# Optimization experiments

Measured on AMD Instinct MI355X. Metric: run time of the kernel, lower is better.

## Reference

```python
import jax, jax.numpy as jnp
import numpy as np

B, L, P, K, D, H = 8192, 224, 6, 5, 128, 4
S = K * K                 # 25 spatial positions in the patch
CENTER = S // 2           # central target pixel index
SCALE_RANGE = 0.2
BN_EPS = 1e-5


def _uniform(k, shape, fan_in):
    s = 1.0 / np.sqrt(fan_in)
    return jax.random.uniform(k, shape, jnp.float32, -s, s)


def setup_inputs() -> dict:
    key = jax.random.key(0)
    ks = jax.random.split(key, 32)
    inp = {}
    inp["x"] = jax.random.normal(ks[0], (B, L, K, K), jnp.float32)
    # attention projections (stored as (in, out), applied as x @ W + b)
    inp["wk_w"] = _uniform(ks[1], (L, D), L); inp["wk_b"] = _uniform(ks[2], (D,), L)
    inp["wv_w"] = _uniform(ks[3], (L, D), L); inp["wv_b"] = _uniform(ks[4], (D,), L)
    inp["wq_w"] = _uniform(ks[5], (L, D), L); inp["wq_b"] = _uniform(ks[6], (D,), L)
    inp["ng_w"] = _uniform(ks[7], (D, 1), D); inp["ng_b"] = _uniform(ks[8], (1,), D)
    # ffn branch: GLU(128->64) -> BN -> GLU(64->P)
    inp["f1_fw"] = _uniform(ks[9], (D, 64), D);  inp["f1_fb"] = _uniform(ks[10], (64,), D)
    inp["f1_gw"] = _uniform(ks[11], (D, 64), D); inp["f1_gb"] = _uniform(ks[12], (64,), D)
    inp["f_bn_g"] = jnp.ones((64,), jnp.float32); inp["f_bn_b"] = jnp.zeros((64,), jnp.float32)
    inp["f2_fw"] = _uniform(ks[13], (64, P), 64); inp["f2_fb"] = _uniform(ks[14], (P,), 64)
    inp["f2_gw"] = _uniform(ks[15], (64, P), 64); inp["f2_gb"] = _uniform(ks[16], (P,), 64)
    # scalar branch: same shapes
    inp["s1_fw"] = _uniform(ks[17], (D, 64), D);  inp["s1_fb"] = _uniform(ks[18], (64,), D)
    inp["s1_gw"] = _uniform(ks[19], (D, 64), D);  inp["s1_gb"] = _uniform(ks[20], (64,), D)
    inp["s_bn_g"] = jnp.ones((64,), jnp.float32); inp["s_bn_b"] = jnp.zeros((64,), jnp.float32)
    inp["s2_fw"] = _uniform(ks[21], (64, P), 64); inp["s2_fb"] = _uniform(ks[22], (P,), 64)
    inp["s2_gw"] = _uniform(ks[23], (64, P), 64); inp["s2_gb"] = _uniform(ks[24], (P,), 64)
    # endmember spectra (P, L), nonnegative as typical for HSI
    inp["endmember"] = jax.random.uniform(ks[25], (P, L), jnp.float32)
    return inp


def _swish(x):
    return x * jax.nn.sigmoid(x)


def _glu(x, fw, fb, gw, gb):
    return (x @ fw + fb) * jax.nn.sigmoid(x @ gw + gb)


def _bn_train(x, g, b):
    # BatchNorm1d training-mode forward: biased batch stats over batch dim
    m = jnp.mean(x, axis=0)
    v = jnp.var(x, axis=0)
    return (x - m) * jax.lax.rsqrt(v + BN_EPS) * g + b


def _forward(x, wk_w, wk_b, wv_w, wv_b, wq_w, wq_b, ng_w, ng_b,
             f1_fw, f1_fb, f1_gw, f1_gb, f_bn_g, f_bn_b, f2_fw, f2_fb, f2_gw, f2_gb,
             s1_fw, s1_fb, s1_gw, s1_gb, s_bn_g, s_bn_b, s2_fw, s2_fb, s2_gw, s2_gb,
             endmember):
    b = x.shape[0]
    xt = x.reshape(b, L, S).transpose(0, 2, 1)        # (B, S, L)
    keys = xt @ wk_w + wk_b                            # (B, S, D)
    vals = xt @ wv_w + wv_b                            # (B, S, D)
    q = xt[:, CENTER] @ wq_w + wq_b                    # (B, D)
    dk, dv = D // H, D // H
    kh = keys.reshape(b, S, H, dk)
    qh = q.reshape(b, H, dk)
    # note: scaling uses full key_dim (np.sqrt(self.key_dim)), not per-head dim
    scores = jnp.einsum('bhd,bshd->bhs', qh, kh) / np.sqrt(D).astype(np.float32)
    mask = jnp.zeros((S,), jnp.float32).at[CENTER].set(-1e6)
    att = jax.nn.softmax(scores + mask, axis=-1)       # (B, H, S)
    vh = vals.reshape(b, S, H, dv)
    surround = jnp.einsum('bhs,bshd->bhd', att, vh).reshape(b, D)
    central = vals[:, CENTER]                          # (B, D)
    nearby = jax.nn.sigmoid((central - surround) @ ng_w + ng_b)  # (B, 1)
    ss = central + nearby * surround                   # (B, D) spatial-spectral feature

    h = _glu(_swish(ss), f1_fw, f1_fb, f1_gw, f1_gb)
    h = _swish(_bn_train(h, f_bn_g, f_bn_b))
    abd = jax.nn.softmax(_glu(h, f2_fw, f2_fb, f2_gw, f2_gb), axis=1)  # (B, P)

    g = _glu(_swish(ss), s1_fw, s1_fb, s1_gw, s1_gb)
    g = _swish(_bn_train(g, s_bn_g, s_bn_b))
    edm_scale = jnp.tanh(_glu(g, s2_fw, s2_fb, s2_gw, s2_gb))          # (B, P)

    scale = 1.0 + SCALE_RANGE * edm_scale[:, :, None]  # (B, P, 1)
    edm = scale * endmember[None]                      # (B, P, L)
    recon = jnp.einsum('bp,bpl->bl', abd, edm)         # (B, L)
    return recon, abd, edm_scale


def reference(x, wk_w, wk_b, wv_w, wv_b, wq_w, wq_b, ng_w, ng_b,
              f1_fw, f1_fb, f1_gw, f1_gb, f_bn_g, f_bn_b, f2_fw, f2_fb, f2_gw, f2_gb,
              s1_fw, s1_fb, s1_gw, s1_gb, s_bn_g, s_bn_b, s2_fw, s2_fb, s2_gw, s2_gb,
              endmember):
    return _forward(x, wk_w, wk_b, wv_w, wv_b, wq_w, wq_b, ng_w, ng_b,
                    f1_fw, f1_fb, f1_gw, f1_gb, f_bn_g, f_bn_b, f2_fw, f2_fb, f2_gw, f2_gb,
                    s1_fw, s1_fb, s1_gw, s1_gb, s_bn_g, s_bn_b, s2_fw, s2_fb, s2_gw, s2_gb,
                    endmember)
```

## Files before the change

kernel.cpp:

```cpp
#include <hip/hip_runtime.h>
#include <hip/hip_bf16.h>

typedef unsigned short ushort;
typedef unsigned int   uint;
typedef __bf16 bfrag_t __attribute__((ext_vector_type(8)));
typedef float  ffrag_t __attribute__((ext_vector_type(4)));

#define NB   8192
#define LL   224
#define SS   25
#define CTR  12
#define DD   128
#define PP   6
#define HID  64
#define GPB  2
#define NKC  7
#define NMT  4
#define NNT  24
#define VST  132
#define VBASE (GPB * SS * VST)
#define WPK_ELEMS (NKC * NNT * 64 * 8)
#define FC1_ELEMS (4 * 16 * 64 * 8)

__device__ __forceinline__ float f_sigmoid(float x) { return 1.0f / (1.0f + __expf(-x)); }
__device__ __forceinline__ ushort f2bf(float f) {
    __hip_bfloat16 h = __float2bfloat16(f);
    ushort u; __builtin_memcpy(&u, &h, 2); return u;
}
__device__ __forceinline__ float bfu2f(ushort u) {
    uint v = ((uint)u) << 16; float f; __builtin_memcpy(&f, &v, 4); return f;
}

__global__ __launch_bounds__(256) void k0_pack(
    const float* __restrict__ wk_w, const float* __restrict__ wv_w,
    const float* __restrict__ wq_w,
    const float* __restrict__ f1_fw, const float* __restrict__ f1_gw,
    const float* __restrict__ s1_fw, const float* __restrict__ s1_gw,
    ushort* __restrict__ wpack, ushort* __restrict__ fc1pack,
    float* __restrict__ stats)
{
    const int blk = blockIdx.x;
    if (blk == 0) stats[threadIdx.x] = 0.f;
    if (blk < NNT) {
        const int nt  = blk;
        const int mat = nt >> 3;
        const float* w = mat == 0 ? wk_w : (mat == 1 ? wv_w : wq_w);
        const int cb = (nt & 7) * 16;
        for (int e = threadIdx.x; e < NKC * 64 * 8; e += 256) {
            int j    = e & 7;
            int lane = (e >> 3) & 63;
            int kc   = e >> 9;
            int k = kc * 32 + ((lane >> 4) << 3) + j;
            int c = cb + (lane & 15);
            wpack[((kc * NNT + nt) * 64 + lane) * 8 + j] = f2bf(w[k * DD + c]);
        }
    } else {
        const int nt = blk - NNT;
        const int m2 = nt >> 2;
        const float* w = m2 == 0 ? f1_fw : (m2 == 1 ? f1_gw : (m2 == 2 ? s1_fw : s1_gw));
        const int cb = (nt & 3) * 16;
        for (int e = threadIdx.x; e < 4 * 64 * 8; e += 256) {
            int j    = e & 7;
            int lane = (e >> 3) & 63;
            int kc   = e >> 9;
            int k = kc * 32 + ((lane >> 4) << 3) + j;
            int c = cb + (lane & 15);
            fc1pack[((kc * 16 + nt) * 64 + lane) * 8 + j] = f2bf(w[k * HID + c]);
        }
    }
}

__global__ __launch_bounds__(512, 4) void kA_front(
    const float* __restrict__ x,
    const ushort* __restrict__ wpack,
    const float* __restrict__ wk_b, const float* __restrict__ wv_b,
    const float* __restrict__ wq_b,
    const float* __restrict__ ng_w, const float* __restrict__ ng_b,
    ushort* __restrict__ swv_ws)
{
    __shared__ ushort alds[NMT * NKC * 64 * 8];
    __shared__ float  qv[GPB * DD];
    __shared__ float  att[8 * 26];
    __shared__ float  red[4];

    const int t    = threadIdx.x;
    const int b0   = blockIdx.x * GPB;
    const int wave = t >> 6;
    const int lane = t & 63;

    const int cC = wave * 16 + (lane & 15);
    const float biask = wk_b[cC];
    const float biasv = wv_b[cC];
    const float biasq = wq_b[cC];
    const float ngw   = ng_w[t & 127];

    const float4* xb4 = (const float4*)(x + (size_t)b0 * (LL * SS));
    float4 xf[6];
#pragma unroll
    for (int k = 0; k < 6; ++k) {
        int q = t + k * 512;
        if (q < 2800) xf[k] = xb4[q];
    }
#pragma unroll
    for (int k = 0; k < 6; ++k) {
        int q = t + k * 512;
        if (q < 2800) {
            int e0 = q * 4;
            int g  = e0 >= 5600;
            int eb0 = e0 - g * 5600;
            int l0 = eb0 / 25;
            int s0 = eb0 - l0 * 25;
#pragma unroll
            for (int c = 0; c < 4; ++c) {
                int s = s0 + c;
                int l = l0;
                if (s >= 25) { s -= 25; ++l; }
                int r = g * 32 + s;
                int idx = (((r >> 4) * NKC + (l >> 5)) * 64 +
                           ((r & 15) | (((l >> 3) & 3) << 4))) * 8 + (l & 7);
                float fv = c == 0 ? xf[k].x : c == 1 ? xf[k].y : c == 2 ? xf[k].z : xf[k].w;
                alds[idx] = f2bf(fv);
            }
        }
    }
    __syncthreads();

    ffrag_t acck[NMT], accv[NMT], accq[2];
#pragma unroll
    for (int mt = 0; mt < NMT; ++mt) {
        acck[mt] = ffrag_t{0.f, 0.f, 0.f, 0.f};
        accv[mt] = ffrag_t{0.f, 0.f, 0.f, 0.f};
    }
    accq[0] = ffrag_t{0.f, 0.f, 0.f, 0.f};
    accq[1] = ffrag_t{0.f, 0.f, 0.f, 0.f};

    bfrag_t bk = *(const bfrag_t*)(wpack + ((0 * NNT + wave) * 64 + lane) * 8);
    bfrag_t bv = *(const bfrag_t*)(wpack + ((0 * NNT + wave + 8) * 64 + lane) * 8);
    bfrag_t bq = *(const bfrag_t*)(wpack + ((0 * NNT + wave + 16) * 64 + lane) * 8);
#pragma unroll
    for (int kc = 0; kc < NKC; ++kc) {
        bfrag_t nbk, nbv, nbq;
        if (kc + 1 < NKC) {
            nbk = *(const bfrag_t*)(wpack + (((kc + 1) * NNT + wave) * 64 + lane) * 8);
            nbv = *(const bfrag_t*)(wpack + (((kc + 1) * NNT + wave + 8) * 64 + lane) * 8);
            nbq = *(const bfrag_t*)(wpack + (((kc + 1) * NNT + wave + 16) * 64 + lane) * 8);
        }
#pragma unroll
        for (int mt = 0; mt < NMT; ++mt) {
            bfrag_t af = *(const bfrag_t*)(alds + ((mt * NKC + kc) * 64 + lane) * 8);
            acck[mt] = __builtin_amdgcn_mfma_f32_16x16x32_bf16(af, bk, acck[mt], 0, 0, 0);
            accv[mt] = __builtin_amdgcn_mfma_f32_16x16x32_bf16(af, bv, accv[mt], 0, 0, 0);
            if ((mt & 1) == 0)
                accq[mt >> 1] = __builtin_amdgcn_mfma_f32_16x16x32_bf16(af, bq, accq[mt >> 1], 0, 0, 0);
        }
        if (kc + 1 < NKC) { bk = nbk; bv = nbv; bq = nbq; }
    }
    __syncthreads();

    {
#pragma unroll
        for (int mt = 0; mt < NMT; ++mt) {
#pragma unroll
            for (int reg = 0; reg < 4; ++reg) {
                int r = mt * 16 + ((lane >> 4) << 2) + reg;
                int g = r >> 5;
                int s = r & 31;
                if (s < SS) {
                    alds[(g * SS + s) * VST + cC]         = f2bf(acck[mt][reg] + biask);
                    alds[VBASE + (g * SS + s) * VST + cC] = f2bf(accv[mt][reg] + biasv);
                }
            }
        }
        if ((lane >> 4) == 3) {
            qv[cC]      = accq[0][0] + biasq;
            qv[DD + cC] = accq[1][0] + biasq;
        }
    }
    __syncthreads();

    {
        const int r    = t >> 6;
        const int g    = r >> 2;
        const int h    = r & 3;
        const int l32  = lane & 31;
        const int half = lane >> 5;
        float part = 0.f;
        if (l32 < SS) {
            const ushort* kr = alds + (g * SS + l32) * VST + h * 32 + half * 16;
            const float*  qr = qv + g * DD + h * 32 + half * 16;
            float a0 = 0.f, a1 = 0.f, a2 = 0.f, a3 = 0.f;
#pragma unroll
            for (int i = 0; i < 16; i += 4) {
                a0 = fmaf(qr[i + 0], bfu2f(kr[i + 0]), a0);
                a1 = fmaf(qr[i + 1], bfu2f(kr[i + 1]), a1);
                a2 = fmaf(qr[i + 2], bfu2f(kr[i + 2]), a2);
                a3 = fmaf(qr[i + 3], bfu2f(kr[i + 3]), a3);
            }
            part = (a0 + a1) + (a2 + a3);
        }
        part += __shfl_xor(part, 32);
        float sc = -1e30f;
        if (l32 < SS) {
            sc = part * 0.088388347648318447f;
            if (l32 == CTR) sc -= 1e6f;
        }
        float mx = sc;
#pragma unroll
        for (int m = 16; m > 0; m >>= 1) mx = fmaxf(mx, __shfl_xor(mx, m, 32));
        float e = __expf(sc - mx);
        float sum = e;
#pragma unroll
        for (int m = 16; m > 0; m >>= 1) sum += __shfl_xor(sum, m, 32);
        if (half == 0 && l32 < SS) att[r * 26 + l32] = e / sum;
    }
    __syncthreads();

    if (t < 256) {
        const int g = t >> 7;
        const int d = t & 127;
        const int h = d >> 5;
        const ushort* vrow = alds + VBASE + g * SS * VST + d;
        const float* arow = att + (g * 4 + h) * 26;
        float s0 = 0.f, s1 = 0.f;
#pragma unroll
        for (int s = 0; s < 24; s += 2) {
            s0 = fmaf(arow[s],     bfu2f(vrow[s * VST]),       s0);
            s1 = fmaf(arow[s + 1], bfu2f(vrow[(s + 1) * VST]), s1);
        }
        float sur = fmaf(arow[24], bfu2f(vrow[24 * VST]), s0 + s1);
        float cen = bfu2f(vrow[CTR * VST]);
        float term = (cen - sur) * ngw;
#pragma unroll
        for (int off = 32; off > 0; off >>= 1) term += __shfl_down(term, off);
        if (lane == 0) red[wave] = term;
        __syncthreads();
        float tot = red[g * 2] + red[g * 2 + 1] + ng_b[0];
        float nearby = f_sigmoid(tot);
        float ssv = cen + nearby * sur;
        float sw  = ssv * f_sigmoid(ssv);
        swv_ws[(size_t)(b0 + g) * DD + d] = f2bf(sw);
    } else {
        __syncthreads();
    }
}

__global__ __launch_bounds__(256) void kC_fc1(
    const ushort* __restrict__ swv_ws,
    const ushort* __restrict__ fc1pack,
    const float* __restrict__ f1_fb, const float* __restrict__ f1_gb,
    const float* __restrict__ s1_fb, const float* __restrict__ s1_gb,
    float* __restrict__ h1_ws, float* __restrict__ g1_ws,
    float* __restrict__ stats)
{
    const int t    = threadIdx.x;
    const int wave = t >> 6;
    const int lane = t & 63;
    const int m0   = blockIdx.x * 32;
    const int c16  = wave * 16 + (lane & 15);

    const float fb1 = f1_fb[c16], gb1 = f1_gb[c16];
    const float fb2 = s1_fb[c16], gb2 = s1_gb[c16];

    ffrag_t acc[4][2];
#pragma unroll
    for (int ni = 0; ni < 4; ++ni)
#pragma unroll
        for (int mt = 0; mt < 2; ++mt) acc[ni][mt] = ffrag_t{0.f, 0.f, 0.f, 0.f};

#pragma unroll
    for (int kc = 0; kc < 4; ++kc) {
        bfrag_t bf[4];
#pragma unroll
        for (int ni = 0; ni < 4; ++ni) {
            int nt = wave + 4 * ni;
            bf[ni] = *(const bfrag_t*)(fc1pack + ((kc * 16 + nt) * 64 + lane) * 8);
        }
#pragma unroll
        for (int mt = 0; mt < 2; ++mt) {
            bfrag_t af = *(const bfrag_t*)(swv_ws +
                (size_t)(m0 + mt * 16 + (lane & 15)) * DD + kc * 32 + ((lane >> 4) << 3));
#pragma unroll
            for (int ni = 0; ni < 4; ++ni)
                acc[ni][mt] = __builtin_amdgcn_mfma_f32_16x16x32_bf16(af, bf[ni], acc[ni][mt], 0, 0, 0);
        }
    }

    float hs = 0.f, hq = 0.f, gs = 0.f, gq = 0.f;
#pragma unroll
    for (int mt = 0; mt < 2; ++mt) {
#pragma unroll
        for (int reg = 0; reg < 4; ++reg) {
            int m = m0 + mt * 16 + ((lane >> 4) << 2) + reg;
            float hv = (acc[0][mt][reg] + fb1) * f_sigmoid(acc[1][mt][reg] + gb1);
            float gv = (acc[2][mt][reg] + fb2) * f_sigmoid(acc[3][mt][reg] + gb2);
            h1_ws[(size_t)m * HID + c16] = hv;
            g1_ws[(size_t)m * HID + c16] = gv;
            hs += hv; hq = fmaf(hv, hv, hq);
            gs += gv; gq = fmaf(gv, gv, gq);
        }
    }
    hs += __shfl_xor(hs, 16); hs += __shfl_xor(hs, 32);
    hq += __shfl_xor(hq, 16); hq += __shfl_xor(hq, 32);
    gs += __shfl_xor(gs, 16); gs += __shfl_xor(gs, 32);
    gq += __shfl_xor(gq, 16); gq += __shfl_xor(gq, 32);
    const int cg = lane >> 4;
    float val = cg == 0 ? hs : cg == 1 ? hq : cg == 2 ? gs : gq;
    atomicAdd(&stats[cg * 64 + c16], val);
}

#define K3G 16
__global__ __launch_bounds__(256) void k3_back(
    const float* __restrict__ h1, const float* __restrict__ g1,
    const float* __restrict__ stats,
    const float* __restrict__ f_bng, const float* __restrict__ f_bnb,
    const float* __restrict__ s_bng, const float* __restrict__ s_bnb,
    const float* __restrict__ f2_fw, const float* __restrict__ f2_fb,
    const float* __restrict__ f2_gw, const float* __restrict__ f2_gb,
    const float* __restrict__ s2_fw, const float* __restrict__ s2_fb,
    const float* __restrict__ s2_gw, const float* __restrict__ s2_gb,
    const float* __restrict__ endm,
    float* __restrict__ out_recon, float* __restrict__ out_abd,
    float* __restrict__ out_es)
{
    const int B0 = blockIdx.x * K3G;
    const int t = threadIdx.x;
    __shared__ float bnl[256];
    __shared__ float w2[4][HID * PP];
    __shared__ float b2[4][8];
    __shared__ float endl[PP * LL];
    __shared__ float hh[K3G * 65], gg[K3G * 65];
    __shared__ float logit[K3G * 8], esv[K3G * 8], coef[K3G * 8];

    if (t < 128) {
        int br = t >> 6, j = t & 63;
        float S1 = stats[br * 128 + j];
        float S2 = stats[br * 128 + 64 + j];
        float m   = S1 * (1.0f / NB);
        float var = S2 * (1.0f / NB) - m * m;
        float gam = br ? s_bng[j] : f_bng[j];
        float be  = br ? s_bnb[j] : f_bnb[j];
        float a   = gam * rsqrtf(var + 1e-5f);
        bnl[br * 128 + j]      = a;
        bnl[br * 128 + 64 + j] = be - m * a;
    }
    for (int i = t; i < HID * PP; i += 256) {
        w2[0][i] = f2_fw[i];
        w2[1][i] = f2_gw[i];
        w2[2][i] = s2_fw[i];
        w2[3][i] = s2_gw[i];
    }
    if (t < PP) {
        b2[0][t] = f2_fb[t];
        b2[1][t] = f2_gb[t];
        b2[2][t] = s2_fb[t];
        b2[3][t] = s2_gb[t];
    }
    for (int i = t; i < PP * LL; i += 256) endl[i] = endm[i];
    __syncthreads();

    for (int i = t; i < K3G * HID; i += 256) {
        int ba = i >> 6, j = i & 63;
        float v1 = h1[(size_t)(B0 + ba) * HID + j] * bnl[j] + bnl[64 + j];
        hh[ba * 65 + j] = v1 * f_sigmoid(v1);
        float v2 = g1[(size_t)(B0 + ba) * HID + j] * bnl[128 + j] + bnl[192 + j];
        gg[ba * 65 + j] = v2 * f_sigmoid(v2);
    }
    __syncthreads();

    for (int i = t; i < K3G * 2 * PP; i += 256) {
        int ba = i / (2 * PP);
        int rr = i - ba * (2 * PP);
        int br = rr / PP;
        int p  = rr - br * PP;
        const float* src = (br ? gg : hh) + ba * 65;
        const float* fw  = w2[br * 2];
        const float* gw  = w2[br * 2 + 1];
        float df = b2[br * 2][p], dg = b2[br * 2 + 1][p];
#pragma unroll 8
        for (int j = 0; j < HID; ++j) {
            float v = src[j];
            df = fmaf(v, fw[j * PP + p], df);
            dg = fmaf(v, gw[j * PP + p], dg);
        }
        float glu = df * f_sigmoid(dg);
        if (br == 0) {
            logit[ba * 8 + p] = glu;
        } else {
            float e = tanhf(glu);
            esv[ba * 8 + p] = e;
            out_es[(size_t)(B0 + ba) * PP + p] = e;
        }
    }
    __syncthreads();

    if (t < K3G) {
        float mx = -1e30f;
#pragma unroll
        for (int p = 0; p < PP; ++p) mx = fmaxf(mx, logit[t * 8 + p]);
        float e[PP]; float sum = 0.f;
#pragma unroll
        for (int p = 0; p < PP; ++p) { e[p] = __expf(logit[t * 8 + p] - mx); sum += e[p]; }
        float inv = 1.0f / sum;
#pragma unroll
        for (int p = 0; p < PP; ++p) {
            float a = e[p] * inv;
            out_abd[(size_t)(B0 + t) * PP + p] = a;
            coef[t * 8 + p] = a * (1.0f + 0.2f * esv[t * 8 + p]);
        }
    }
    __syncthreads();

    for (int i = t; i < K3G * LL; i += 256) {
        int ba = i / LL;
        int l  = i - ba * LL;
        float r = 0.f;
#pragma unroll
        for (int p = 0; p < PP; ++p)
            r = fmaf(coef[ba * 8 + p], endl[p * LL + l], r);
        out_recon[(size_t)(B0 + ba) * LL + l] = r;
    }
}

extern "C" void kernel_launch(void* const* d_in, const int* in_sizes, int n_in,
                              void* d_out, int out_size, void* d_ws, size_t ws_size,
                              hipStream_t stream)
{
    const float* x     = (const float*)d_in[0];
    const float* wk_w  = (const float*)d_in[1];
    const float* wk_b  = (const float*)d_in[2];
    const float* wv_w  = (const float*)d_in[3];
    const float* wv_b  = (const float*)d_in[4];
    const float* wq_w  = (const float*)d_in[5];
    const float* wq_b  = (const float*)d_in[6];
    const float* ng_w  = (const float*)d_in[7];
    const float* ng_b  = (const float*)d_in[8];
    const float* f1_fw = (const float*)d_in[9];
    const float* f1_fb = (const float*)d_in[10];
    const float* f1_gw = (const float*)d_in[11];
    const float* f1_gb = (const float*)d_in[12];
    const float* f_bng = (const float*)d_in[13];
    const float* f_bnb = (const float*)d_in[14];
    const float* f2_fw = (const float*)d_in[15];
    const float* f2_fb = (const float*)d_in[16];
    const float* f2_gw = (const float*)d_in[17];
    const float* f2_gb = (const float*)d_in[18];
    const float* s1_fw = (const float*)d_in[19];
    const float* s1_fb = (const float*)d_in[20];
    const float* s1_gw = (const float*)d_in[21];
    const float* s1_gb = (const float*)d_in[22];
    const float* s_bng = (const float*)d_in[23];
    const float* s_bnb = (const float*)d_in[24];
    const float* s2_fw = (const float*)d_in[25];
    const float* s2_fb = (const float*)d_in[26];
    const float* s2_gw = (const float*)d_in[27];
    const float* s2_gb = (const float*)d_in[28];
    const float* endm  = (const float*)d_in[29];

    float* ws = (float*)d_ws;
    float*  h1_ws   = ws;
    float*  g1_ws   = ws + (size_t)NB * HID;
    float*  stats   = ws + 1048576;
    ushort* wpack   = (ushort*)(ws + 1048832);
    ushort* fc1pack = (ushort*)(ws + 1048832 + WPK_ELEMS / 2);
    ushort* swv_ws  = (ushort*)(ws + 1048832 + (WPK_ELEMS + FC1_ELEMS) / 2);

    float* out       = (float*)d_out;
    float* out_recon = out;
    float* out_abd   = out + (size_t)NB * LL;
    float* out_es    = out + (size_t)NB * (LL + PP);

    k0_pack<<<NNT + 16, 256, 0, stream>>>(wk_w, wv_w, wq_w, f1_fw, f1_gw,
                                          s1_fw, s1_gw, wpack, fc1pack, stats);
    kA_front<<<NB / GPB, 512, 0, stream>>>(x, wpack, wk_b, wv_b, wq_b,
                                           ng_w, ng_b, swv_ws);
    kC_fc1<<<NB / 32, 256, 0, stream>>>(swv_ws, fc1pack, f1_fb, f1_gb,
                                        s1_fb, s1_gb, h1_ws, g1_ws, stats);
    k3_back<<<NB / K3G, 256, 0, stream>>>(h1_ws, g1_ws, stats,
                                          f_bng, f_bnb, s_bng, s_bnb,
                                          f2_fw, f2_fb, f2_gw, f2_gb,
                                          s2_fw, s2_fb, s2_gw, s2_gb,
                                          endm, out_recon, out_abd, out_es);
}
```

Before: 365.2 us.

## Process one batch item per 256-thread block with two column tiles per wave

The front attention kernel now handles one sample per block with 4 waves instead of two samples with 8 waves. Each wave computes two 16-column N tiles for K, V and Q over 2 M tiles, so each A fragment load feeds more MFMAs. The software prefetch of the next B fragment is replaced by direct loads inside the loop. This aims for smaller blocks and better occupancy, but wastes more of the M padding (25 rows padded to 32 per sample) and doubles the block count.

```diff
diff --git a/kernel.cpp b/kernel.cpp
--- a/kernel.cpp
+++ b/kernel.cpp
@@ -13,12 +13,11 @@
 #define DD   128
 #define PP   6
 #define HID  64
-#define GPB  2
 #define NKC  7
-#define NMT  4
+#define NMT  2
 #define NNT  24
 #define VST  132
-#define VBASE (GPB * SS * VST)
+#define VBASE (SS * VST)
 #define WPK_ELEMS (NKC * NNT * 64 * 8)
 #define FC1_ELEMS (4 * 16 * 64 * 8)
 
@@ -70,7 +69,7 @@
     }
 }
 
-__global__ __launch_bounds__(512, 4) void kA_front(
+__global__ __launch_bounds__(256, 4) void kA_front(
     const float* __restrict__ x,
     const ushort* __restrict__ wpack,
     const float* __restrict__ wk_b, const float* __restrict__ wv_b,
@@ -79,45 +78,42 @@
     ushort* __restrict__ swv_ws)
 {
     __shared__ ushort alds[NMT * NKC * 64 * 8];
-    __shared__ float  qv[GPB * DD];
-    __shared__ float  att[8 * 26];
-    __shared__ float  red[4];
+    __shared__ float  qv[DD];
+    __shared__ float  att[4 * 26];
+    __shared__ float  red[2];
 
     const int t    = threadIdx.x;
-    const int b0   = blockIdx.x * GPB;
     const int wave = t >> 6;
     const int lane = t & 63;
 
-    const int cC = wave * 16 + (lane & 15);
-    const float biask = wk_b[cC];
-    const float biasv = wv_b[cC];
-    const float biasq = wq_b[cC];
-    const float ngw   = ng_w[t & 127];
-
-    const float4* xb4 = (const float4*)(x + (size_t)b0 * (LL * SS));
+    const int c0 = wave * 16 + (lane & 15);
+    const int c1 = c0 + 64;
+    const float biask0 = wk_b[c0], biask1 = wk_b[c1];
+    const float biasv0 = wv_b[c0], biasv1 = wv_b[c1];
+    const float biasq0 = wq_b[c0], biasq1 = wq_b[c1];
+    const float ngw    = ng_w[t & 127];
+
+    const float4* xb4 = (const float4*)(x + (size_t)blockIdx.x * (LL * SS));
     float4 xf[6];
 #pragma unroll
     for (int k = 0; k < 6; ++k) {
-        int q = t + k * 512;
-        if (q < 2800) xf[k] = xb4[q];
+        int q = t + k * 256;
+        if (q < 1400) xf[k] = xb4[q];
     }
 #pragma unroll
     for (int k = 0; k < 6; ++k) {
-        int q = t + k * 512;
-        if (q < 2800) {
+        int q = t + k * 256;
+        if (q < 1400) {
             int e0 = q * 4;
-            int g  = e0 >= 5600;
-            int eb0 = e0 - g * 5600;
-            int l0 = eb0 / 25;
-            int s0 = eb0 - l0 * 25;
+            int l0 = e0 / 25;
+            int s0 = e0 - l0 * 25;
 #pragma unroll
             for (int c = 0; c < 4; ++c) {
                 int s = s0 + c;
                 int l = l0;
                 if (s >= 25) { s -= 25; ++l; }
-                int r = g * 32 + s;
-                int idx = (((r >> 4) * NKC + (l >> 5)) * 64 +
-                           ((r & 15) | (((l >> 3) & 3) << 4))) * 8 + (l & 7);
+                int idx = (((s >> 4) * NKC + (l >> 5)) * 64 +
+                           ((s & 15) | (((l >> 3) & 3) << 4))) * 8 + (l & 7);
                 float fv = c == 0 ? xf[k].x : c == 1 ? xf[k].y : c == 2 ? xf[k].z : xf[k].w;
                 alds[idx] = f2bf(fv);
             }
@@ -125,69 +121,73 @@
     }
     __syncthreads();
 
-    ffrag_t acck[NMT], accv[NMT], accq[2];
-#pragma unroll
-    for (int mt = 0; mt < NMT; ++mt) {
-        acck[mt] = ffrag_t{0.f, 0.f, 0.f, 0.f};
-        accv[mt] = ffrag_t{0.f, 0.f, 0.f, 0.f};
-    }
+    ffrag_t acck[2][NMT], accv[2][NMT], accq[2];
+#pragma unroll
+    for (int ti = 0; ti < 2; ++ti)
+#pragma unroll
+        for (int mt = 0; mt < NMT; ++mt) {
+            acck[ti][mt] = ffrag_t{0.f, 0.f, 0.f, 0.f};
+            accv[ti][mt] = ffrag_t{0.f, 0.f, 0.f, 0.f};
+        }
     accq[0] = ffrag_t{0.f, 0.f, 0.f, 0.f};
     accq[1] = ffrag_t{0.f, 0.f, 0.f, 0.f};
 
-    bfrag_t bk = *(const bfrag_t*)(wpack + ((0 * NNT + wave) * 64 + lane) * 8);
-    bfrag_t bv = *(const bfrag_t*)(wpack + ((0 * NNT + wave + 8) * 64 + lane) * 8);
-    bfrag_t bq = *(const bfrag_t*)(wpack + ((0 * NNT + wave + 16) * 64 + lane) * 8);
 #pragma unroll
     for (int kc = 0; kc < NKC; ++kc) {
-        bfrag_t nbk, nbv, nbq;
-        if (kc + 1 < NKC) {
-            nbk = *(const bfrag_t*)(wpack + (((kc + 1) * NNT + wave) * 64 + lane) * 8);
-            nbv = *(const bfrag_t*)(wpack + (((kc + 1) * NNT + wave + 8) * 64 + lane) * 8);
-            nbq = *(const bfrag_t*)(wpack + (((kc + 1) * NNT + wave + 16) * 64 + lane) * 8);
-        }
-#pragma unroll
-        for (int mt = 0; mt < NMT; ++mt) {
-            bfrag_t af = *(const bfrag_t*)(alds + ((mt * NKC + kc) * 64 + lane) * 8);
-            acck[mt] = __builtin_amdgcn_mfma_f32_16x16x32_bf16(af, bk, acck[mt], 0, 0, 0);
-            accv[mt] = __builtin_amdgcn_mfma_f32_16x16x32_bf16(af, bv, accv[mt], 0, 0, 0);
-            if ((mt & 1) == 0)
-                accq[mt >> 1] = __builtin_amdgcn_mfma_f32_16x16x32_bf16(af, bq, accq[mt >> 1], 0, 0, 0);
-        }
-        if (kc + 1 < NKC) { bk = nbk; bv = nbv; bq = nbq; }
+        bfrag_t bk0 = *(const bfrag_t*)(wpack + ((kc * NNT + wave)      * 64 + lane) * 8);
+        bfrag_t bk1 = *(const bfrag_t*)(wpack + ((kc * NNT + wave + 4)  * 64 + lane) * 8);
+        bfrag_t bv0 = *(const bfrag_t*)(wpack + ((kc * NNT + wave + 8)  * 64 + lane) * 8);
+        bfrag_t bv1 = *(const bfrag_t*)(wpack + ((kc * NNT + wave + 12) * 64 + lane) * 8);
+        bfrag_t bq0 = *(const bfrag_t*)(wpack + ((kc * NNT + wave + 16) * 64 + lane) * 8);
+        bfrag_t bq1 = *(const bfrag_t*)(wpack + ((kc * NNT + wave + 20) * 64 + lane) * 8);
+        bfrag_t af0 = *(const bfrag_t*)(alds + ((0 * NKC + kc) * 64 + lane) * 8);
+        bfrag_t af1 = *(const bfrag_t*)(alds + ((1 * NKC + kc) * 64 + lane) * 8);
+        acck[0][0] = __builtin_amdgcn_mfma_f32_16x16x32_bf16(af0, bk0, acck[0][0], 0, 0, 0);
+        acck[0][1] = __builtin_amdgcn_mfma_f32_16x16x32_bf16(af1, bk0, acck[0][1], 0, 0, 0);
+        acck[1][0] = __builtin_amdgcn_mfma_f32_16x16x32_bf16(af0, bk1, acck[1][0], 0, 0, 0);
+        acck[1][1] = __builtin_amdgcn_mfma_f32_16x16x32_bf16(af1, bk1, acck[1][1], 0, 0, 0);
+        accv[0][0] = __builtin_amdgcn_mfma_f32_16x16x32_bf16(af0, bv0, accv[0][0], 0, 0, 0);
+        accv[0][1] = __builtin_amdgcn_mfma_f32_16x16x32_bf16(af1, bv0, accv[0][1], 0, 0, 0);
+        accv[1][0] = __builtin_amdgcn_mfma_f32_16x16x32_bf16(af0, bv1, accv[1][0], 0, 0, 0);
+        accv[1][1] = __builtin_amdgcn_mfma_f32_16x16x32_bf16(af1, bv1, accv[1][1], 0, 0, 0);
+        accq[0]    = __builtin_amdgcn_mfma_f32_16x16x32_bf16(af0, bq0, accq[0],    0, 0, 0);
+        accq[1]    = __builtin_amdgcn_mfma_f32_16x16x32_bf16(af0, bq1, accq[1],    0, 0, 0);
     }
     __syncthreads();
 
     {
 #pragma unroll
-        for (int mt = 0; mt < NMT; ++mt) {
-#pragma unroll
-            for (int reg = 0; reg < 4; ++reg) {
-                int r = mt * 16 + ((lane >> 4) << 2) + reg;
-                int g = r >> 5;
-                int s = r & 31;
-                if (s < SS) {
-                    alds[(g * SS + s) * VST + cC]         = f2bf(acck[mt][reg] + biask);
-                    alds[VBASE + (g * SS + s) * VST + cC] = f2bf(accv[mt][reg] + biasv);
+        for (int ti = 0; ti < 2; ++ti) {
+            const int   col = ti ? c1 : c0;
+            const float bk  = ti ? biask1 : biask0;
+            const float bv  = ti ? biasv1 : biasv0;
+#pragma unroll
+            for (int mt = 0; mt < NMT; ++mt) {
+#pragma unroll
+                for (int reg = 0; reg < 4; ++reg) {
+                    int s = mt * 16 + ((lane >> 4) << 2) + reg;
+                    if (s < SS) {
+                        alds[s * VST + col]         = f2bf(acck[ti][mt][reg] + bk);
+                        alds[VBASE + s * VST + col] = f2bf(accv[ti][mt][reg] + bv);
+                    }
                 }
             }
         }
         if ((lane >> 4) == 3) {
-            qv[cC]      = accq[0][0] + biasq;
-            qv[DD + cC] = accq[1][0] + biasq;
+            qv[c0] = accq[0][0] + biasq0;
+            qv[c1] = accq[1][0] + biasq1;
         }
     }
     __syncthreads();
 
     {
-        const int r    = t >> 6;
-        const int g    = r >> 2;
-        const int h    = r & 3;
+        const int h    = wave;
         const int l32  = lane & 31;
         const int half = lane >> 5;
         float part = 0.f;
         if (l32 < SS) {
-            const ushort* kr = alds + (g * SS + l32) * VST + h * 32 + half * 16;
-            const float*  qr = qv + g * DD + h * 32 + half * 16;
+            const ushort* kr = alds + l32 * VST + h * 32 + half * 16;
+            const float*  qr = qv + h * 32 + half * 16;
             float a0 = 0.f, a1 = 0.f, a2 = 0.f, a3 = 0.f;
 #pragma unroll
             for (int i = 0; i < 16; i += 4) {
@@ -211,36 +211,36 @@
         float sum = e;
 #pragma unroll
         for (int m = 16; m > 0; m >>= 1) sum += __shfl_xor(sum, m, 32);
-        if (half == 0 && l32 < SS) att[r * 26 + l32] = e / sum;
-    }
-    __syncthreads();
-
-    if (t < 256) {
-        const int g = t >> 7;
-        const int d = t & 127;
+        if (half == 0 && l32 < SS) att[h * 26 + l32] = e / sum;
+    }
+    __syncthreads();
+
+    float sur = 0.f, cen = 0.f;
+    if (t < 128) {
+        const int d = t;
         const int h = d >> 5;
-        const ushort* vrow = alds + VBASE + g * SS * VST + d;
-        const float* arow = att + (g * 4 + h) * 26;
+        const ushort* vrow = alds + VBASE + d;
+        const float* arow = att + h * 26;
         float s0 = 0.f, s1 = 0.f;
 #pragma unroll
         for (int s = 0; s < 24; s += 2) {
             s0 = fmaf(arow[s],     bfu2f(vrow[s * VST]),       s0);
             s1 = fmaf(arow[s + 1], bfu2f(vrow[(s + 1) * VST]), s1);
         }
-        float sur = fmaf(arow[24], bfu2f(vrow[24 * VST]), s0 + s1);
-        float cen = bfu2f(vrow[CTR * VST]);
+        sur = fmaf(arow[24], bfu2f(vrow[24 * VST]), s0 + s1);
+        cen = bfu2f(vrow[CTR * VST]);
         float term = (cen - sur) * ngw;
 #pragma unroll
         for (int off = 32; off > 0; off >>= 1) term += __shfl_down(term, off);
         if (lane == 0) red[wave] = term;
-        __syncthreads();
-        float tot = red[g * 2] + red[g * 2 + 1] + ng_b[0];
+    }
+    __syncthreads();
+    if (t < 128) {
+        float tot = red[0] + red[1] + ng_b[0];
         float nearby = f_sigmoid(tot);
         float ssv = cen + nearby * sur;
         float sw  = ssv * f_sigmoid(ssv);
-        swv_ws[(size_t)(b0 + g) * DD + d] = f2bf(sw);
-    } else {
-        __syncthreads();
+        swv_ws[(size_t)blockIdx.x * DD + t] = f2bf(sw);
     }
 }
 
@@ -471,8 +471,8 @@
 
     k0_pack<<<NNT + 16, 256, 0, stream>>>(wk_w, wv_w, wq_w, f1_fw, f1_gw,
                                           s1_fw, s1_gw, wpack, fc1pack, stats);
-    kA_front<<<NB / GPB, 512, 0, stream>>>(x, wpack, wk_b, wv_b, wq_b,
-                                           ng_w, ng_b, swv_ws);
+    kA_front<<<NB, 256, 0, stream>>>(x, wpack, wk_b, wv_b, wq_b,
+                                     ng_w, ng_b, swv_ws);
     kC_fc1<<<NB / 32, 256, 0, stream>>>(swv_ws, fc1pack, f1_fb, f1_gb,
                                         s1_fb, s1_gb, h1_ws, g1_ws, stats);
     k3_back<<<NB / K3G, 256, 0, stream>>>(h1_ws, g1_ws, stats,
```

Measured after the change: 386.2 us. +5.8%, slower.
